# Performance work log

Measured on AMD Instinct MI355X. Metric: run time of the kernel, lower is better.

Reference implementation:

```python
import jax, jax.numpy as jnp
import numpy as np

V, D, R = 100000, 128, 20000  # vocab size, embed dim, number of residual (trainable) rows
B, S = 64, 4096               # batch, seq_len


def setup_inputs() -> dict:
    key = jax.random.key(0)
    k1, k2 = jax.random.split(key)
    pretrained_embedding = jax.random.normal(k1, (V, D), dtype=jnp.float32)
    # distinct vocab ids chosen as residual/trainable rows (torch builds a dict id -> row)
    ridx = np.sort(np.random.default_rng(0).permutation(V)[:R]).astype(np.int64)
    residual_index = jnp.asarray(ridx)
    # torch init: residual_embedding = pretrained_embedding.index_select(0, residual_index)
    residual_embedding = pretrained_embedding[residual_index]
    x = jax.random.randint(k2, (B, S), 0, V, dtype=jnp.int64)
    return {
        "x": x,
        "residual_index": residual_index,
        "pretrained_embedding": pretrained_embedding,
        "residual_embedding": residual_embedding,
    }


def reference(x, residual_index, pretrained_embedding, residual_embedding):
    # remap[v] = position of v in residual_index, else -1 (vectorized form of the torch dict)
    num_res = residual_index.shape[0]
    remap = jnp.full((pretrained_embedding.shape[0],), -1, dtype=jnp.int32)
    remap = remap.at[residual_index].set(jnp.arange(num_res, dtype=jnp.int32))
    r = remap[x]                    # [B, S] residual row or -1
    use_residual = r >= 0           # [B, S]
    res_rows = residual_embedding[jnp.maximum(r, 0)]   # [B, S, D]
    pre_rows = pretrained_embedding[x]                 # [B, S, D]
    return jnp.where(use_residual[..., None], res_rows, pre_rows)
```

## Files before the change

kernel.cpp:

```cpp
#include <hip/hip_runtime.h>


#define BLOCK 256
#define UNROLL 2

typedef __attribute__((ext_vector_type(4))) float f4;

__global__ void fill_remap_kernel(int* __restrict__ remap, int V) {
    int i = blockIdx.x * blockDim.x + threadIdx.x;
    if (i < V) remap[i] = -1;
}

__global__ void scatter_remap_kernel(int* __restrict__ remap,
                                     const int* __restrict__ ridx, int R) {
    int i = blockIdx.x * blockDim.x + threadIdx.x;
    if (i < R) remap[ridx[i]] = i;
}

__global__ void resolve_kernel(const int* __restrict__ x,
                               const int* __restrict__ remap,
                               int* __restrict__ combined, int n_tokens) {
    int i = blockIdx.x * blockDim.x + threadIdx.x;
    if (i >= n_tokens) return;
    int t = x[i];
    int r = remap[t];
    combined[i] = (r >= 0) ? (int)(0x80000000u | (unsigned)r) : t;
}

__global__ __launch_bounds__(BLOCK, 8) void gather_kernel(
        const int* __restrict__ combined,
        const f4* __restrict__ pre,
        const f4* __restrict__ res,
        f4* __restrict__ out,
        int n_tokens, int n_groups) {
    int g    = (blockIdx.x * BLOCK + threadIdx.x) >> 5;
    int lane = threadIdx.x & 31;

    int tok[UNROLL];
    const f4* src[UNROLL];
    bool ok[UNROLL];

    #pragma unroll
    for (int k = 0; k < UNROLL; ++k) {
        tok[k] = g + k * n_groups;
        ok[k]  = tok[k] < n_tokens;
        if (ok[k]) {
            int c = combined[tok[k]];
            src[k] = (c < 0) ? res + (size_t)(c & 0x7fffffff) * 32
                             : pre + (size_t)c * 32;
        }
    }

    f4 val[UNROLL];
    #pragma unroll
    for (int k = 0; k < UNROLL; ++k)
        if (ok[k]) val[k] = src[k][lane];

    #pragma unroll
    for (int k = 0; k < UNROLL; ++k)
        if (ok[k])
            __builtin_nontemporal_store(val[k],
                &out[(size_t)tok[k] * 32 + lane]);
}

extern "C" void kernel_launch(void* const* d_in, const int* in_sizes, int n_in,
                              void* d_out, int out_size, void* d_ws, size_t ws_size,
                              hipStream_t stream) {
    const int* x    = (const int*)d_in[0];
    const int* ridx = (const int*)d_in[1];
    const f4*  pre  = (const f4*)d_in[2];
    const f4*  res  = (const f4*)d_in[3];
    f4*        out  = (f4*)d_out;

    const int n_tokens = in_sizes[0];
    const int R        = in_sizes[1];
    const int D        = in_sizes[3] / R;
    const int V        = in_sizes[2] / D;
    (void)ws_size;

    int* remap    = (int*)d_ws;
    int* combined = remap + V;

    fill_remap_kernel<<<(V + 255) / 256, 256, 0, stream>>>(remap, V);
    scatter_remap_kernel<<<(R + 255) / 256, 256, 0, stream>>>(remap, ridx, R);
    resolve_kernel<<<(n_tokens + 255) / 256, 256, 0, stream>>>(x, remap,
                                                               combined,
                                                               n_tokens);

    int n_groups = (n_tokens + UNROLL - 1) / UNROLL;
    int threads  = n_groups * 32;
    int blocks   = (threads + BLOCK - 1) / BLOCK;
    gather_kernel<<<blocks, BLOCK, 0, stream>>>(combined, pre, res, out,
                                                n_tokens, n_groups);
}
```

Before: 205.4 us.

## Replace remap table with per-token binary search over sorted residual index

Removes the fill, scatter and resolve kernels and their workspace traffic. Each gather warp instead binary-searches the sorted residual_index for its token id and picks the residual or pretrained row directly. This cuts three launches and the remap/combined memory passes, but adds about 15 dependent global loads per token. Correctness depends on residual_index being sorted, which the setup guarantees.

After: 259.8 us. 1.27x slower.

```diff
diff --git a/kernel.cpp b/kernel.cpp
--- a/kernel.cpp
+++ b/kernel.cpp
@@ -6,49 +6,40 @@
 
 typedef __attribute__((ext_vector_type(4))) float f4;
 
-__global__ void fill_remap_kernel(int* __restrict__ remap, int V) {
-    int i = blockIdx.x * blockDim.x + threadIdx.x;
-    if (i < V) remap[i] = -1;
-}
-
-__global__ void scatter_remap_kernel(int* __restrict__ remap,
-                                     const int* __restrict__ ridx, int R) {
-    int i = blockIdx.x * blockDim.x + threadIdx.x;
-    if (i < R) remap[ridx[i]] = i;
-}
-
-__global__ void resolve_kernel(const int* __restrict__ x,
-                               const int* __restrict__ remap,
-                               int* __restrict__ combined, int n_tokens) {
-    int i = blockIdx.x * blockDim.x + threadIdx.x;
-    if (i >= n_tokens) return;
-    int t = x[i];
-    int r = remap[t];
-    combined[i] = (r >= 0) ? (int)(0x80000000u | (unsigned)r) : t;
-}
-
-__global__ __launch_bounds__(BLOCK, 8) void gather_kernel(
-        const int* __restrict__ combined,
+__global__ __launch_bounds__(BLOCK, 8) void fused_gather_kernel(
+        const int* __restrict__ x,
+        const int* __restrict__ ridx,
         const f4* __restrict__ pre,
         const f4* __restrict__ res,
         f4* __restrict__ out,
-        int n_tokens, int n_groups) {
+        int n_tokens, int n_groups, int R, int step0) {
     int g    = (blockIdx.x * BLOCK + threadIdx.x) >> 5;
     int lane = threadIdx.x & 31;
 
-    int tok[UNROLL];
-    const f4* src[UNROLL];
+    int tok[UNROLL], t[UNROLL];
     bool ok[UNROLL];
-
     #pragma unroll
     for (int k = 0; k < UNROLL; ++k) {
         tok[k] = g + k * n_groups;
         ok[k]  = tok[k] < n_tokens;
-        if (ok[k]) {
-            int c = combined[tok[k]];
-            src[k] = (c < 0) ? res + (size_t)(c & 0x7fffffff) * 32
-                             : pre + (size_t)c * 32;
+        t[k]   = ok[k] ? x[tok[k]] : 0;
+    }
+
+    int lo[UNROLL] = {0};
+    for (int step = step0; step > 0; step >>= 1) {
+        #pragma unroll
+        for (int k = 0; k < UNROLL; ++k) {
+            int cand = lo[k] + step;
+            if (cand <= R && ridx[cand - 1] < t[k]) lo[k] = cand;
         }
+    }
+
+    const f4* src[UNROLL];
+    #pragma unroll
+    for (int k = 0; k < UNROLL; ++k) {
+        bool hit = (lo[k] < R) && (ridx[lo[k]] == t[k]);
+        src[k] = hit ? res + (size_t)lo[k] * 32
+                     : pre + (size_t)t[k] * 32;
     }
 
     f4 val[UNROLL];
@@ -74,22 +65,15 @@
 
     const int n_tokens = in_sizes[0];
     const int R        = in_sizes[1];
-    const int D        = in_sizes[3] / R;
-    const int V        = in_sizes[2] / D;
-    (void)ws_size;
+    (void)n_in; (void)out_size; (void)d_ws; (void)ws_size;
 
-    int* remap    = (int*)d_ws;
-    int* combined = remap + V;
-
-    fill_remap_kernel<<<(V + 255) / 256, 256, 0, stream>>>(remap, V);
-    scatter_remap_kernel<<<(R + 255) / 256, 256, 0, stream>>>(remap, ridx, R);
-    resolve_kernel<<<(n_tokens + 255) / 256, 256, 0, stream>>>(x, remap,
-                                                               combined,
-                                                               n_tokens);
+    int step0 = 1;
+    while ((step0 << 1) <= R) step0 <<= 1;
 
     int n_groups = (n_tokens + UNROLL - 1) / UNROLL;
     int threads  = n_groups * 32;
     int blocks   = (threads + BLOCK - 1) / BLOCK;
-    gather_kernel<<<blocks, BLOCK, 0, stream>>>(combined, pre, res, out,
-                                                n_tokens, n_groups);
+    fused_gather_kernel<<<blocks, BLOCK, 0, stream>>>(x, ridx, pre, res, out,
+                                                      n_tokens, n_groups, R,
+                                                      step0);
 }
```
